# Kernel optimization log

Measured on AMD Instinct MI355X. Metric: run time of the kernel, lower is better.

Reference implementation:

```python
import jax, jax.numpy as jnp
import numpy as np

N = 20000   # nodes
E = 320000  # edges (avg degree 16)
K = 3       # Chebyshev order


def _glorot(key, shape):
    fan_in, fan_out = shape[-2], shape[-1]
    lim = (6.0 / (fan_in + fan_out)) ** 0.5
    return jax.random.uniform(key, shape, minval=-lim, maxval=lim, dtype=jnp.float32)


def setup_inputs() -> dict:
    key = jax.random.key(0)
    ks = jax.random.split(key, 8)
    v = jax.random.normal(ks[0], (N, 86), dtype=jnp.float32)
    edges = jax.random.randint(ks[1], (2, E), 0, N, dtype=jnp.int32)
    W1 = _glorot(ks[2], (K, 86, 128));  b1 = jnp.zeros((128,), jnp.float32)
    W2 = _glorot(ks[3], (K, 128, 256)); b2 = jnp.zeros((256,), jnp.float32)
    W3 = _glorot(ks[4], (K, 256, 512)); b3 = jnp.zeros((512,), jnp.float32)
    return {"v": v, "edges": edges, "W1": W1, "b1": b1,
            "W2": W2, "b2": b2, "W3": W3, "b3": b3}


def _cheb_norm(edges, n):
    # PyG ChebConv with sym norm, lambda_max=2: L_hat = L - I = -D^-1/2 A D^-1/2
    # (diagonal entries from get_laplacian (+1) and add_self_loops (-1) cancel).
    # Self loops are removed before computing the Laplacian -> mask them out.
    row, col = edges[0], edges[1]
    w = (row != col).astype(jnp.float32)
    deg = jax.ops.segment_sum(w, row, num_segments=n)
    dinv = jnp.where(deg > 0, jax.lax.rsqrt(jnp.maximum(deg, 1e-12)), 0.0)
    norm_w = -dinv[row] * w * dinv[col]  # [E]
    return row, col, norm_w


def _cheb_conv(x, row, col, norm_w, W, b):
    # W: [K, in, out]
    def prop(z):  # L_hat @ z via edge gather + segment scatter-add
        return jax.ops.segment_sum(norm_w[:, None] * z[col], row, num_segments=x.shape[0])
    Tx0 = x
    out = Tx0 @ W[0]
    Tx1 = prop(Tx0)
    out = out + Tx1 @ W[1]
    Tx2 = 2.0 * prop(Tx1) - Tx0
    out = out + Tx2 @ W[2]
    return out + b


def reference(v, edges, W1, b1, W2, b2, W3, b3):
    row, col, norm_w = _cheb_norm(edges, v.shape[0])
    nk = jax.random.key(42)
    x1 = jax.nn.relu(_cheb_conv(v, row, col, norm_w, W1, b1))
    x1 = x1 * jax.random.normal(jax.random.fold_in(nk, 1), x1.shape, x1.dtype)
    x2 = jax.nn.relu(_cheb_conv(x1, row, col, norm_w, W2, b2))
    x2 = x2 * jax.random.normal(jax.random.fold_in(nk, 2), x2.shape, x2.dtype)
    x3 = jax.nn.relu(_cheb_conv(x2, row, col, norm_w, W3, b3))
    x3 = x3 * jax.random.normal(jax.random.fold_in(nk, 3), x3.shape, x3.dtype)
    return (x1, x2, x3)
```

## Files before the change

kernel.cpp:

```cpp
#include <hip/hip_runtime.h>
#include <stdint.h>
#include <math.h>

#define DEV static __device__ __forceinline__

typedef __attribute__((ext_vector_type(8))) short bf16x8;
typedef __attribute__((ext_vector_type(4))) float f32x4;
typedef __attribute__((ext_vector_type(8))) unsigned short u16x8;

DEV uint32_t rotl32(uint32_t v, int d) { return (v << d) | (v >> (32 - d)); }

DEV void threefry2x32(uint32_t k0, uint32_t k1, uint32_t& x0, uint32_t& x1) {
  const uint32_t k2 = k0 ^ k1 ^ 0x1BD11BDAu;
  x0 += k0; x1 += k1;
#define TFR(R) { x0 += x1; x1 = rotl32(x1, R) ^ x0; }
  TFR(13) TFR(15) TFR(26) TFR(6)
  x0 += k1; x1 += k2 + 1u;
  TFR(17) TFR(29) TFR(16) TFR(24)
  x0 += k2; x1 += k0 + 2u;
  TFR(13) TFR(15) TFR(26) TFR(6)
  x0 += k0; x1 += k1 + 3u;
  TFR(17) TFR(29) TFR(16) TFR(24)
  x0 += k1; x1 += k2 + 4u;
  TFR(13) TFR(15) TFR(26) TFR(6)
  x0 += k2; x1 += k0 + 5u;
#undef TFR
}

DEV float erfinv_f32(float x) {
  float w = -log1pf(-x * x);
  float p;
  if (w < 5.0f) {
    w -= 2.5f;
    p = 2.81022636e-08f;
    p = fmaf(p, w, 3.43273939e-07f);
    p = fmaf(p, w, -3.5233877e-06f);
    p = fmaf(p, w, -4.39150654e-06f);
    p = fmaf(p, w, 0.00021858087f);
    p = fmaf(p, w, -0.00125372503f);
    p = fmaf(p, w, -0.00417768164f);
    p = fmaf(p, w, 0.246640727f);
    p = fmaf(p, w, 1.50140941f);
  } else {
    w = sqrtf(w) - 3.0f;
    p = -0.000200214257f;
    p = fmaf(p, w, 0.000100950558f);
    p = fmaf(p, w, 0.00134934322f);
    p = fmaf(p, w, -0.00367342844f);
    p = fmaf(p, w, 0.00573950773f);
    p = fmaf(p, w, -0.0076224613f);
    p = fmaf(p, w, 0.00943887047f);
    p = fmaf(p, w, 1.00167406f);
    p = fmaf(p, w, 2.83297682f);
  }
  return p * x;
}

DEV float normal_from_bits(uint32_t bits) {
  float f = __uint_as_float((bits >> 9) | 0x3F800000u) - 1.0f;
  const float lo = -0.99999994f;
  float u = fmaf(f, 2.0f, lo);
  u = fmaxf(u, lo);
  return 1.41421356f * erfinv_f32(u);
}

DEV unsigned short f2bf(float f) {
  uint32_t u = __float_as_uint(f);
  uint32_t r = u + 0x7FFFu + ((u >> 16) & 1u);
  return (unsigned short)(r >> 16);
}

DEV float bf2f(uint32_t h) { return __uint_as_float(h << 16); }

DEV float4 noise4(uint32_t f0, uint32_t f1, uint32_t i4) {
  uint32_t base = i4 * 4u;
  float4 r;
  { uint32_t a = 0u, b = base + 0u; threefry2x32(f0, f1, a, b); r.x = normal_from_bits(a ^ b); }
  { uint32_t a = 0u, b = base + 1u; threefry2x32(f0, f1, a, b); r.y = normal_from_bits(a ^ b); }
  { uint32_t a = 0u, b = base + 2u; threefry2x32(f0, f1, a, b); r.z = normal_from_bits(a ^ b); }
  { uint32_t a = 0u, b = base + 3u; threefry2x32(f0, f1, a, b); r.w = normal_from_bits(a ^ b); }
  return r;
}

DEV void noise_fill(unsigned short* __restrict__ nb, int total4, int fold,
                    int gbase, int gstride) {
  uint32_t f0k = 0u, f1k = (uint32_t)fold;
  threefry2x32(0u, 42u, f0k, f1k);
  for (int i4 = gbase; i4 < total4; i4 += gstride) {
    float4 r = noise4(f0k, f1k, (uint32_t)i4);
    uint2 u;
    u.x = (uint32_t)f2bf(r.x) | ((uint32_t)f2bf(r.y) << 16);
    u.y = (uint32_t)f2bf(r.z) | ((uint32_t)f2bf(r.w) << 16);
    *(uint2*)&nb[(size_t)i4 * 4] = u;
  }
}

__global__ void count_kernel(const int* __restrict__ rows, const int* __restrict__ cols,
                             int* __restrict__ counts, int* __restrict__ degs, int E) {
  int e = blockIdx.x * blockDim.x + threadIdx.x;
  if (e < E) {
    int r = rows[e];
    atomicAdd(&counts[r], 1);
    if (r != cols[e]) atomicAdd(&degs[r], 1);
  }
}

#define SCAN_T 1024
__global__ __launch_bounds__(SCAN_T) void scan_kernel(const int* __restrict__ counts,
                                                      int* __restrict__ row_ptr,
                                                      int* __restrict__ cursor, int N) {
  __shared__ int sa[SCAN_T], sb[SCAN_T];
  const int t = threadIdx.x;
  const int CH = (N + SCAN_T - 1) / SCAN_T;
  int base = t * CH;
  int psum = 0;
  for (int k = 0; k < CH; ++k) {
    int idx = base + k;
    if (idx < N) psum += counts[idx];
  }
  sa[t] = psum;
  __syncthreads();
  int* src = sa; int* dst = sb;
  for (int off = 1; off < SCAN_T; off <<= 1) {
    int v = src[t];
    if (t >= off) v += src[t - off];
    dst[t] = v;
    __syncthreads();
    int* tmp = src; src = dst; dst = tmp;
  }
  int running = src[t] - psum;
  for (int k = 0; k < CH; ++k) {
    int idx = base + k;
    if (idx < N) {
      row_ptr[idx] = running;
      cursor[idx] = running;
      running += counts[idx];
    }
  }
  if (t == SCAN_T - 1) row_ptr[N] = running;
}

__global__ void fill_kernel(const int* __restrict__ rows, const int* __restrict__ cols,
                            const int* __restrict__ degs, int* __restrict__ cursor,
                            float2* __restrict__ ecv, int E) {
  int e = blockIdx.x * blockDim.x + threadIdx.x;
  if (e < E) {
    int r = rows[e], c = cols[e];
    int dr = degs[r], dc = degs[c];
    float w = (r != c && dr > 0 && dc > 0) ? -rsqrtf((float)dr) * rsqrtf((float)dc) : 0.0f;
    int pos = atomicAdd(&cursor[r], 1);
    ecv[pos] = make_float2(__int_as_float(c), w);
  }
}

__global__ void prep_kernel(const float* __restrict__ v,
                            const float* __restrict__ W1, const float* __restrict__ W2,
                            const float* __restrict__ W3,
                            unsigned short* __restrict__ vb, unsigned short* __restrict__ wt1,
                            unsigned short* __restrict__ wt2, unsigned short* __restrict__ wt3,
                            unsigned short* __restrict__ nb1, int n1_total4, int N) {
  noise_fill(nb1, n1_total4, 1, blockIdx.x * 256 + threadIdx.x, gridDim.x * 256);

  int i = blockIdx.x * 256 + threadIdx.x;
  int nv = N * 96;
  if (i < nv) {
    int r = i / 96, k = i % 96;
    vb[i] = (k < 86) ? f2bf(v[(size_t)r * 86 + k]) : (unsigned short)0;
    return;
  }
  i -= nv;
  if (i < 3 * 128 * 96) {
    int k = i % 96, o = (i / 96) % 128, p = i / (96 * 128);
    float val = 0.0f;
    if (k < 86) {
      if (p == 0)      val = W1[((size_t)0 * 86 + k) * 128 + o] - W1[((size_t)2 * 86 + k) * 128 + o];
      else if (p == 1) val = W1[((size_t)1 * 86 + k) * 128 + o];
      else             val = 2.0f * W1[((size_t)2 * 86 + k) * 128 + o];
    }
    wt1[i] = (k < 86) ? f2bf(val) : (unsigned short)0;
    return;
  }
  i -= 3 * 128 * 96;
  if (i < 3 * 256 * 128) {
    int k = i % 128, o = (i / 128) % 256, p = i / (128 * 256);
    float val;
    if (p == 0)      val = W2[((size_t)0 * 128 + k) * 256 + o] - W2[((size_t)2 * 128 + k) * 256 + o];
    else if (p == 1) val = W2[((size_t)1 * 128 + k) * 256 + o];
    else             val = 2.0f * W2[((size_t)2 * 128 + k) * 256 + o];
    wt2[i] = f2bf(val);
    return;
  }
  i -= 3 * 256 * 128;
  if (i < 3 * 512 * 256) {
    int k = i % 256, o = (i / 256) % 512, p = i / (256 * 512);
    float val;
    if (p == 0)      val = W3[((size_t)0 * 256 + k) * 512 + o] - W3[((size_t)2 * 256 + k) * 512 + o];
    else if (p == 1) val = W3[((size_t)1 * 256 + k) * 512 + o];
    else             val = 2.0f * W3[((size_t)2 * 256 + k) * 512 + o];
    wt3[i] = f2bf(val);
  }
}

DEV void ld8(const unsigned short* __restrict__ base, size_t off, float* v) {
  uint4 u = *(const uint4*)(base + off);
  v[0] = bf2f(u.x & 0xffffu); v[1] = bf2f(u.x >> 16);
  v[2] = bf2f(u.y & 0xffffu); v[3] = bf2f(u.y >> 16);
  v[4] = bf2f(u.z & 0xffffu); v[5] = bf2f(u.z >> 16);
  v[6] = bf2f(u.w & 0xffffu); v[7] = bf2f(u.w >> 16);
}

template <int LPN, int NL>
__global__ __launch_bounds__(256) void gather_prop(
    const int* __restrict__ row_ptr, const float2* __restrict__ ecv,
    const unsigned short* __restrict__ xsrc, int sstride,
    unsigned short* __restrict__ outb, int N, int Fpad) {
  const int wave = threadIdx.x >> 6, lane = threadIdx.x & 63;
  const int sub = lane / LPN;
  const int fl = (lane - sub * LPN) * 8;
  const int node = (blockIdx.x * 4 + wave) * NL + sub;
  if (sub >= NL || node >= N) return;
  float acc[8] = {};
  const int s = row_ptr[node], e = row_ptr[node + 1];
  int j = s;
  for (; j + 8 <= e; j += 8) {
    float2 cw[8];
    float vv[8][8];
#pragma unroll
    for (int q = 0; q < 8; ++q) cw[q] = ecv[j + q];
#pragma unroll
    for (int q = 0; q < 8; ++q)
      ld8(xsrc, (size_t)__float_as_int(cw[q].x) * sstride + fl, vv[q]);
#pragma unroll
    for (int q = 0; q < 8; ++q)
#pragma unroll
      for (int z = 0; z < 8; ++z) acc[z] = fmaf(cw[q].y, vv[q][z], acc[z]);
  }
  for (; j + 2 <= e; j += 2) {
    float2 cw[2];
    float vv[2][8];
#pragma unroll
    for (int q = 0; q < 2; ++q) cw[q] = ecv[j + q];
#pragma unroll
    for (int q = 0; q < 2; ++q)
      ld8(xsrc, (size_t)__float_as_int(cw[q].x) * sstride + fl, vv[q]);
#pragma unroll
    for (int q = 0; q < 2; ++q)
#pragma unroll
      for (int z = 0; z < 8; ++z) acc[z] = fmaf(cw[q].y, vv[q][z], acc[z]);
  }
  for (; j < e; ++j) {
    float2 cw = ecv[j];
    float vv[8];
    ld8(xsrc, (size_t)__float_as_int(cw.x) * sstride + fl, vv);
#pragma unroll
    for (int z = 0; z < 8; ++z) acc[z] = fmaf(cw.y, vv[z], acc[z]);
  }
  uint4 u;
  u.x = (uint32_t)f2bf(acc[0]) | ((uint32_t)f2bf(acc[1]) << 16);
  u.y = (uint32_t)f2bf(acc[2]) | ((uint32_t)f2bf(acc[3]) << 16);
  u.z = (uint32_t)f2bf(acc[4]) | ((uint32_t)f2bf(acc[5]) << 16);
  u.w = (uint32_t)f2bf(acc[6]) | ((uint32_t)f2bf(acc[7]) << 16);
  *(uint4*)&outb[(size_t)node * Fpad + fl] = u;
}

template <int BM, int FPAD, int KS, int OB>
__global__ __launch_bounds__(512, 4) void gemm3_db(
    const unsigned short* __restrict__ A0, const unsigned short* __restrict__ A1,
    const unsigned short* __restrict__ A2,
    const unsigned short* __restrict__ Wt, const float* __restrict__ bias,
    const unsigned short* __restrict__ noise,
    int M, int MT, int O, float* __restrict__ out, unsigned short* __restrict__ outb,
    int obstride, unsigned short* __restrict__ nnext, int ntotal4, int nfold) {
  constexpr int BN = 128;
  constexpr int NSP = FPAD / KS;
  constexpr int NSTEP = 3 * NSP;
  constexpr int CPR = KS / 8;
  constexpr int LST = KS + 8;
  constexpr int NA = BM * CPR;
  constexpr int NB = BN * CPR;
  constexpr int ACH = (NA + 511) / 512;
  constexpr int BCH = (NB + 511) / 512;
  constexpr int MFR = BM / 32;
  constexpr int KK = KS / 32;

  const int flat = blockIdx.x;
  const int xcd = flat & 7, idx = flat >> 3;
  const int mtile = xcd + 8 * (idx / OB);
  const int obl = idx - (idx / OB) * OB;

  __shared__ unsigned short sA[2][BM * LST];
  __shared__ unsigned short sB[2][BN * LST];

  const int tid = threadIdx.x;

  if (mtile < MT) {
    const int bm = mtile * BM;
    const int bo = obl * BN;
    const int lane = tid & 63;
    const int wave = tid >> 6;
    const int wm = wave >> 2, wo = wave & 3;
    const int l15 = lane & 15;
    const int kg = (lane >> 4) * 8;

    f32x4 acc[MFR][2] = {};
    const unsigned short* As[3] = {A0, A1, A2};

    u16x8 ra0[ACH], rb0[BCH], ra1[ACH], rb1[BCH];

    auto issue = [&](int s, u16x8 (&ra)[ACH], u16x8 (&rb)[BCH]) {
      int p = s / NSP, k0 = (s % NSP) * KS;
      const unsigned short* __restrict__ A = As[p];
      const unsigned short* __restrict__ B = Wt + (size_t)p * O * FPAD;
#pragma unroll
      for (int c = 0; c < ACH; ++c) {
        int idx2 = tid + c * 512;
        if (NA % 512 == 0 || idx2 < NA) {
          int row = idx2 / CPR, ch = (idx2 % CPR) * 8;
          int gm = bm + row; if (gm >= M) gm = M - 1;
          ra[c] = *(const u16x8*)(A + (size_t)gm * FPAD + k0 + ch);
        }
      }
#pragma unroll
      for (int c = 0; c < BCH; ++c) {
        int idx2 = tid + c * 512;
        if (NB % 512 == 0 || idx2 < NB) {
          int row = idx2 / CPR, ch = (idx2 % CPR) * 8;
          rb[c] = *(const u16x8*)(B + (size_t)(bo + row) * FPAD + k0 + ch);
        }
      }
    };

    auto lds_write = [&](int buf, u16x8 (&ra)[ACH], u16x8 (&rb)[BCH]) {
#pragma unroll
      for (int c = 0; c < ACH; ++c) {
        int idx2 = tid + c * 512;
        if (NA % 512 == 0 || idx2 < NA) {
          int row = idx2 / CPR, ch = (idx2 % CPR) * 8;
          *(u16x8*)&sA[buf][row * LST + ch] = ra[c];
        }
      }
#pragma unroll
      for (int c = 0; c < BCH; ++c) {
        int idx2 = tid + c * 512;
        if (NB % 512 == 0 || idx2 < NB) {
          int row = idx2 / CPR, ch = (idx2 % CPR) * 8;
          *(u16x8*)&sB[buf][row * LST + ch] = rb[c];
        }
      }
    };

    auto compute = [&](int buf) {
#pragma unroll
      for (int kk = 0; kk < KK; ++kk) {
        bf16x8 af[MFR], bfr[2];
#pragma unroll
        for (int mi = 0; mi < MFR; ++mi)
          af[mi] = *(const bf16x8*)&sA[buf][(wm * (BM / 2) + mi * 16 + l15) * LST + kk * 32 + kg];
#pragma unroll
        for (int ni = 0; ni < 2; ++ni)
          bfr[ni] = *(const bf16x8*)&sB[buf][(wo * 32 + ni * 16 + l15) * LST + kk * 32 + kg];
#pragma unroll
        for (int mi = 0; mi < MFR; ++mi)
#pragma unroll
          for (int ni = 0; ni < 2; ++ni)
            acc[mi][ni] = __builtin_amdgcn_mfma_f32_16x16x32_bf16(af[mi], bfr[ni], acc[mi][ni], 0, 0, 0);
      }
    };

    issue(0, ra0, rb0);
    issue(1, ra1, rb1);
    lds_write(0, ra0, rb0);
    __syncthreads();

#pragma unroll
    for (int s = 0; s < NSTEP; ++s) {
      if ((s & 1) == 0) {
        if (s + 2 < NSTEP) issue(s + 2, ra0, rb0);
        compute(s & 1);
        if (s + 1 < NSTEP) { lds_write((s + 1) & 1, ra1, rb1); __syncthreads(); }
      } else {
        if (s + 2 < NSTEP) issue(s + 2, ra1, rb1);
        compute(s & 1);
        if (s + 1 < NSTEP) { lds_write((s + 1) & 1, ra0, rb0); __syncthreads(); }
      }
    }

    const int r0 = (lane >> 4) * 4;
#pragma unroll
    for (int mi = 0; mi < MFR; ++mi) {
#pragma unroll
      for (int r = 0; r < 4; ++r) {
        int gm = bm + wm * (BM / 2) + mi * 16 + r0 + r;
        if (gm >= M) continue;
#pragma unroll
        for (int ni = 0; ni < 2; ++ni) {
          int go = bo + wo * 32 + ni * 16 + l15;
          float vv = acc[mi][ni][r] + bias[go];
          vv = vv > 0.0f ? vv : 0.0f;
          float res = vv * bf2f((uint32_t)noise[(size_t)gm * O + go]);
          out[(size_t)gm * O + go] = res;
          if (outb) outb[(size_t)gm * obstride + go] = f2bf(res);
        }
      }
    }
  }

  if (nnext)
    noise_fill(nnext, ntotal4, nfold, blockIdx.x * 512 + tid, gridDim.x * 512);
}

extern "C" void kernel_launch(void* const* d_in, const int* in_sizes, int n_in,
                              void* d_out, int out_size, void* d_ws, size_t ws_size,
                              hipStream_t stream) {
  const float* v    = (const float*)d_in[0];
  const int*  edges = (const int*)d_in[1];
  const float* W1 = (const float*)d_in[2];
  const float* b1 = (const float*)d_in[3];
  const float* W2 = (const float*)d_in[4];
  const float* b2 = (const float*)d_in[5];
  const float* W3 = (const float*)d_in[6];
  const float* b3 = (const float*)d_in[7];
  float* out = (float*)d_out;

  const int N = in_sizes[0] / 86;
  const int E = in_sizes[1] / 2;
  const int* rows = edges;
  const int* cols = edges + E;

  uintptr_t cur = (uintptr_t)d_ws;
  auto alloc = [&](size_t bytes) {
    cur = (cur + 15) & ~(uintptr_t)15;
    void* p = (void*)cur;
    cur += bytes;
    return p;
  };
  float2* ecv          = (float2*)alloc((size_t)E * 8);
  int* counts          = (int*)alloc((size_t)N * 4);
  int* degs            = (int*)alloc((size_t)N * 4);
  int* row_ptr         = (int*)alloc((size_t)(N + 1) * 4);
  int* cursor          = (int*)alloc((size_t)N * 4);
  unsigned short* tx1b = (unsigned short*)alloc((size_t)N * 256 * 2);
  unsigned short* tx2b = (unsigned short*)alloc((size_t)N * 256 * 2);
  unsigned short* vb   = (unsigned short*)alloc((size_t)N * 96 * 2);
  unsigned short* x1b  = (unsigned short*)alloc((size_t)N * 128 * 2);
  unsigned short* x2b  = (unsigned short*)alloc((size_t)N * 256 * 2);
  unsigned short* wt1  = (unsigned short*)alloc((size_t)3 * 128 * 96 * 2);
  unsigned short* wt2  = (unsigned short*)alloc((size_t)3 * 256 * 128 * 2);
  unsigned short* wt3  = (unsigned short*)alloc((size_t)3 * 512 * 256 * 2);
  unsigned short* nb2  = (unsigned short*)alloc((size_t)N * 256 * 2);
  unsigned short* nb3  = (unsigned short*)alloc((size_t)N * 512 * 2);
  unsigned short* nb1  = nb3;

  float* x1 = out;
  float* x2 = x1 + (size_t)N * 128;
  float* x3 = x2 + (size_t)N * 256;

  hipMemsetAsync(counts, 0, (size_t)2 * N * sizeof(int), stream);
  count_kernel<<<(E + 255) / 256, 256, 0, stream>>>(rows, cols, counts, degs, E);
  scan_kernel<<<1, SCAN_T, 0, stream>>>(counts, row_ptr, cursor, N);
  fill_kernel<<<(E + 255) / 256, 256, 0, stream>>>(rows, cols, degs, cursor, ecv, E);
  {
    int total = N * 96 + 3 * 128 * 96 + 3 * 256 * 128 + 3 * 512 * 256;
    prep_kernel<<<(total + 255) / 256, 256, 0, stream>>>(v, W1, W2, W3, vb, wt1, wt2, wt3,
                                                         nb1, N * 128 / 4, N);
  }

  {
    int pb = (N + 15) / 16;
    gather_prop<12, 4><<<pb, 256, 0, stream>>>(row_ptr, ecv, vb, 96, tx1b, N, 96);
    gather_prop<12, 4><<<pb, 256, 0, stream>>>(row_ptr, ecv, tx1b, 96, tx2b, N, 96);
    int mt = (N + 63) / 64;
    int grid = 8 * ((mt + 7) / 8) * 1;
    gemm3_db<64, 96, 32, 1><<<grid, 512, 0, stream>>>(vb, tx1b, tx2b, wt1, b1, nb1,
                                                      N, mt, 128, x1, x1b, 128,
                                                      nb2, N * 256 / 4, 2);
  }
  {
    int pb = (N + 15) / 16;
    gather_prop<16, 4><<<pb, 256, 0, stream>>>(row_ptr, ecv, x1b, 128, tx1b, N, 128);
    gather_prop<16, 4><<<pb, 256, 0, stream>>>(row_ptr, ecv, tx1b, 128, tx2b, N, 128);
    int mt = (N + 127) / 128;
    int grid = 8 * ((mt + 7) / 8) * 2;
    gemm3_db<128, 128, 64, 2><<<grid, 512, 0, stream>>>(x1b, tx1b, tx2b, wt2, b2, nb2,
                                                        N, mt, 256, x2, x2b, 256,
                                                        nb3, N * 512 / 4, 3);
  }
  {
    int pb = (N + 7) / 8;
    gather_prop<32, 2><<<pb, 256, 0, stream>>>(row_ptr, ecv, x2b, 256, tx1b, N, 256);
    gather_prop<32, 2><<<pb, 256, 0, stream>>>(row_ptr, ecv, tx1b, 256, tx2b, N, 256);
    int mt = (N + 127) / 128;
    int grid = 8 * ((mt + 7) / 8) * 4;
    gemm3_db<128, 256, 64, 4><<<grid, 512, 0, stream>>>(x2b, tx1b, tx2b, wt3, b3, nb3,
                                                        N, mt, 512, x3, nullptr, 0,
                                                        nullptr, 0, 0);
  }
}
```

Before: 416.4 us.

## Move noise generation into gather kernels and slice gathers by feature per XCD

Noise generation for each layer moves out of prep and the previous GEMM's tail into the two memory-bound gather kernels of that layer, each filling half the buffer. The intent is to overlap the ALU-heavy threefry work with gather memory latency and shorten the GEMMs. The layer-2 and layer-3 gathers get a new kernel that maps 64-feature slices to XCDs, so each XCD's L2 holds only a column slice of the source features. The risk is extra ALU load on the gathers, plus occupancy effects.

Measured after the change: 369.0 us. 11.4% less time.

```diff
diff --git a/kernel.cpp b/kernel.cpp
--- a/kernel.cpp
+++ b/kernel.cpp
@@ -82,11 +82,11 @@
   return r;
 }
 
-DEV void noise_fill(unsigned short* __restrict__ nb, int total4, int fold,
+DEV void noise_fill(unsigned short* __restrict__ nb, int n4_begin, int n4_end, int fold,
                     int gbase, int gstride) {
   uint32_t f0k = 0u, f1k = (uint32_t)fold;
   threefry2x32(0u, 42u, f0k, f1k);
-  for (int i4 = gbase; i4 < total4; i4 += gstride) {
+  for (int i4 = n4_begin + gbase; i4 < n4_end; i4 += gstride) {
     float4 r = noise4(f0k, f1k, (uint32_t)i4);
     uint2 u;
     u.x = (uint32_t)f2bf(r.x) | ((uint32_t)f2bf(r.y) << 16);
@@ -158,9 +158,7 @@
                             const float* __restrict__ W3,
                             unsigned short* __restrict__ vb, unsigned short* __restrict__ wt1,
                             unsigned short* __restrict__ wt2, unsigned short* __restrict__ wt3,
-                            unsigned short* __restrict__ nb1, int n1_total4, int N) {
-  noise_fill(nb1, n1_total4, 1, blockIdx.x * 256 + threadIdx.x, gridDim.x * 256);
-
+                            int N) {
   int i = blockIdx.x * 256 + threadIdx.x;
   int nv = N * 96;
   if (i < nv) {
@@ -209,17 +207,9 @@
   v[6] = bf2f(u.w & 0xffffu); v[7] = bf2f(u.w >> 16);
 }
 
-template <int LPN, int NL>
-__global__ __launch_bounds__(256) void gather_prop(
-    const int* __restrict__ row_ptr, const float2* __restrict__ ecv,
-    const unsigned short* __restrict__ xsrc, int sstride,
-    unsigned short* __restrict__ outb, int N, int Fpad) {
-  const int wave = threadIdx.x >> 6, lane = threadIdx.x & 63;
-  const int sub = lane / LPN;
-  const int fl = (lane - sub * LPN) * 8;
-  const int node = (blockIdx.x * 4 + wave) * NL + sub;
-  if (sub >= NL || node >= N) return;
-  float acc[8] = {};
+DEV void gather_node(const int* __restrict__ row_ptr, const float2* __restrict__ ecv,
+                     const unsigned short* __restrict__ xsrc, int sstride, int fl,
+                     int node, float* acc) {
   const int s = row_ptr[node], e = row_ptr[node + 1];
   int j = s;
   for (; j + 8 <= e; j += 8) {
@@ -255,12 +245,57 @@
 #pragma unroll
     for (int z = 0; z < 8; ++z) acc[z] = fmaf(cw.y, vv[z], acc[z]);
   }
+}
+
+DEV void store8(unsigned short* __restrict__ outb, size_t ob, const float* acc) {
   uint4 u;
   u.x = (uint32_t)f2bf(acc[0]) | ((uint32_t)f2bf(acc[1]) << 16);
   u.y = (uint32_t)f2bf(acc[2]) | ((uint32_t)f2bf(acc[3]) << 16);
   u.z = (uint32_t)f2bf(acc[4]) | ((uint32_t)f2bf(acc[5]) << 16);
   u.w = (uint32_t)f2bf(acc[6]) | ((uint32_t)f2bf(acc[7]) << 16);
-  *(uint4*)&outb[(size_t)node * Fpad + fl] = u;
+  *(uint4*)&outb[ob] = u;
+}
+
+template <int LPN, int NL, int FOLD>
+__global__ __launch_bounds__(256) void gather_prop(
+    const int* __restrict__ row_ptr, const float2* __restrict__ ecv,
+    const unsigned short* __restrict__ xsrc, int sstride,
+    unsigned short* __restrict__ outb, int N, int Fpad,
+    unsigned short* __restrict__ nbuf, int n4_begin, int n4_end) {
+  const int wave = threadIdx.x >> 6, lane = threadIdx.x & 63;
+  const int sub = lane / LPN;
+  const int fl = (lane - sub * LPN) * 8;
+  const int node = (blockIdx.x * 4 + wave) * NL + sub;
+  if (sub < NL && node < N && fl < Fpad) {
+    float acc[8] = {};
+    gather_node(row_ptr, ecv, xsrc, sstride, fl, node, acc);
+    store8(outb, (size_t)node * Fpad + fl, acc);
+  }
+  noise_fill(nbuf, n4_begin, n4_end, FOLD, blockIdx.x * 256 + (int)threadIdx.x, gridDim.x * 256);
+}
+
+template <int G, int FOLD>
+__global__ __launch_bounds__(256) void gather_prop_sl(
+    const int* __restrict__ row_ptr, const float2* __restrict__ ecv,
+    const unsigned short* __restrict__ xsrc, int sstride,
+    unsigned short* __restrict__ outb, int N, int Fpad, int NBK,
+    unsigned short* __restrict__ nbuf, int n4_begin, int n4_end) {
+  const int flat = blockIdx.x;
+  const int xcd = flat & 7, j = flat >> 3;
+  const int slice = xcd / G;
+  const int nb = j * G + (xcd % G);
+  if (nb < NBK) {
+    const int wave = threadIdx.x >> 6, lane = threadIdx.x & 63;
+    const int sub = lane >> 3;
+    const int fl = slice * 64 + (lane & 7) * 8;
+    const int node = nb * 32 + wave * 8 + sub;
+    if (node < N) {
+      float acc[8] = {};
+      gather_node(row_ptr, ecv, xsrc, sstride, fl, node, acc);
+      store8(outb, (size_t)node * Fpad + fl, acc);
+    }
+  }
+  noise_fill(nbuf, n4_begin, n4_end, FOLD, flat * 256 + (int)threadIdx.x, gridDim.x * 256);
 }
 
 template <int BM, int FPAD, int KS, int OB>
@@ -270,7 +305,7 @@
     const unsigned short* __restrict__ Wt, const float* __restrict__ bias,
     const unsigned short* __restrict__ noise,
     int M, int MT, int O, float* __restrict__ out, unsigned short* __restrict__ outb,
-    int obstride, unsigned short* __restrict__ nnext, int ntotal4, int nfold) {
+    int obstride) {
   constexpr int BN = 128;
   constexpr int NSP = FPAD / KS;
   constexpr int NSTEP = 3 * NSP;
@@ -287,126 +322,121 @@
   const int xcd = flat & 7, idx = flat >> 3;
   const int mtile = xcd + 8 * (idx / OB);
   const int obl = idx - (idx / OB) * OB;
+  if (mtile >= MT) return;
+  const int bm = mtile * BM;
+  const int bo = obl * BN;
 
   __shared__ unsigned short sA[2][BM * LST];
   __shared__ unsigned short sB[2][BN * LST];
 
   const int tid = threadIdx.x;
-
-  if (mtile < MT) {
-    const int bm = mtile * BM;
-    const int bo = obl * BN;
-    const int lane = tid & 63;
-    const int wave = tid >> 6;
-    const int wm = wave >> 2, wo = wave & 3;
-    const int l15 = lane & 15;
-    const int kg = (lane >> 4) * 8;
-
-    f32x4 acc[MFR][2] = {};
-    const unsigned short* As[3] = {A0, A1, A2};
-
-    u16x8 ra0[ACH], rb0[BCH], ra1[ACH], rb1[BCH];
-
-    auto issue = [&](int s, u16x8 (&ra)[ACH], u16x8 (&rb)[BCH]) {
-      int p = s / NSP, k0 = (s % NSP) * KS;
-      const unsigned short* __restrict__ A = As[p];
-      const unsigned short* __restrict__ B = Wt + (size_t)p * O * FPAD;
-#pragma unroll
-      for (int c = 0; c < ACH; ++c) {
-        int idx2 = tid + c * 512;
-        if (NA % 512 == 0 || idx2 < NA) {
-          int row = idx2 / CPR, ch = (idx2 % CPR) * 8;
-          int gm = bm + row; if (gm >= M) gm = M - 1;
-          ra[c] = *(const u16x8*)(A + (size_t)gm * FPAD + k0 + ch);
-        }
+  const int lane = tid & 63;
+  const int wave = tid >> 6;
+  const int wm = wave >> 2, wo = wave & 3;
+  const int l15 = lane & 15;
+  const int kg = (lane >> 4) * 8;
+
+  f32x4 acc[MFR][2] = {};
+  const unsigned short* As[3] = {A0, A1, A2};
+
+  u16x8 ra0[ACH], rb0[BCH], ra1[ACH], rb1[BCH];
+
+  auto issue = [&](int s, u16x8 (&ra)[ACH], u16x8 (&rb)[BCH]) {
+    int p = s / NSP, k0 = (s % NSP) * KS;
+    const unsigned short* __restrict__ A = As[p];
+    const unsigned short* __restrict__ B = Wt + (size_t)p * O * FPAD;
+#pragma unroll
+    for (int c = 0; c < ACH; ++c) {
+      int idx2 = tid + c * 512;
+      if (NA % 512 == 0 || idx2 < NA) {
+        int row = idx2 / CPR, ch = (idx2 % CPR) * 8;
+        int gm = bm + row; if (gm >= M) gm = M - 1;
+        ra[c] = *(const u16x8*)(A + (size_t)gm * FPAD + k0 + ch);
       }
-#pragma unroll
-      for (int c = 0; c < BCH; ++c) {
-        int idx2 = tid + c * 512;
-        if (NB % 512 == 0 || idx2 < NB) {
-          int row = idx2 / CPR, ch = (idx2 % CPR) * 8;
-          rb[c] = *(const u16x8*)(B + (size_t)(bo + row) * FPAD + k0 + ch);
-        }
+    }
+#pragma unroll
+    for (int c = 0; c < BCH; ++c) {
+      int idx2 = tid + c * 512;
+      if (NB % 512 == 0 || idx2 < NB) {
+        int row = idx2 / CPR, ch = (idx2 % CPR) * 8;
+        rb[c] = *(const u16x8*)(B + (size_t)(bo + row) * FPAD + k0 + ch);
       }
-    };
-
-    auto lds_write = [&](int buf, u16x8 (&ra)[ACH], u16x8 (&rb)[BCH]) {
-#pragma unroll
-      for (int c = 0; c < ACH; ++c) {
-        int idx2 = tid + c * 512;
-        if (NA % 512 == 0 || idx2 < NA) {
-          int row = idx2 / CPR, ch = (idx2 % CPR) * 8;
-          *(u16x8*)&sA[buf][row * LST + ch] = ra[c];
-        }
+    }
+  };
+
+  auto lds_write = [&](int buf, u16x8 (&ra)[ACH], u16x8 (&rb)[BCH]) {
+#pragma unroll
+    for (int c = 0; c < ACH; ++c) {
+      int idx2 = tid + c * 512;
+      if (NA % 512 == 0 || idx2 < NA) {
+        int row = idx2 / CPR, ch = (idx2 % CPR) * 8;
+        *(u16x8*)&sA[buf][row * LST + ch] = ra[c];
       }
-#pragma unroll
-      for (int c = 0; c < BCH; ++c) {
-        int idx2 = tid + c * 512;
-        if (NB % 512 == 0 || idx2 < NB) {
-          int row = idx2 / CPR, ch = (idx2 % CPR) * 8;
-          *(u16x8*)&sB[buf][row * LST + ch] = rb[c];
-        }
+    }
+#pragma unroll
+    for (int c = 0; c < BCH; ++c) {
+      int idx2 = tid + c * 512;
+      if (NB % 512 == 0 || idx2 < NB) {
+        int row = idx2 / CPR, ch = (idx2 % CPR) * 8;
+        *(u16x8*)&sB[buf][row * LST + ch] = rb[c];
       }
-    };
-
-    auto compute = [&](int buf) {
-#pragma unroll
-      for (int kk = 0; kk < KK; ++kk) {
-        bf16x8 af[MFR], bfr[2];
-#pragma unroll
-        for (int mi = 0; mi < MFR; ++mi)
-          af[mi] = *(const bf16x8*)&sA[buf][(wm * (BM / 2) + mi * 16 + l15) * LST + kk * 32 + kg];
+    }
+  };
+
+  auto compute = [&](int buf) {
+#pragma unroll
+    for (int kk = 0; kk < KK; ++kk) {
+      bf16x8 af[MFR], bfr[2];
+#pragma unroll
+      for (int mi = 0; mi < MFR; ++mi)
+        af[mi] = *(const bf16x8*)&sA[buf][(wm * (BM / 2) + mi * 16 + l15) * LST + kk * 32 + kg];
+#pragma unroll
+      for (int ni = 0; ni < 2; ++ni)
+        bfr[ni] = *(const bf16x8*)&sB[buf][(wo * 32 + ni * 16 + l15) * LST + kk * 32 + kg];
+#pragma unroll
+      for (int mi = 0; mi < MFR; ++mi)
 #pragma unroll
         for (int ni = 0; ni < 2; ++ni)
-          bfr[ni] = *(const bf16x8*)&sB[buf][(wo * 32 + ni * 16 + l15) * LST + kk * 32 + kg];
-#pragma unroll
-        for (int mi = 0; mi < MFR; ++mi)
-#pragma unroll
-          for (int ni = 0; ni < 2; ++ni)
-            acc[mi][ni] = __builtin_amdgcn_mfma_f32_16x16x32_bf16(af[mi], bfr[ni], acc[mi][ni], 0, 0, 0);
+          acc[mi][ni] = __builtin_amdgcn_mfma_f32_16x16x32_bf16(af[mi], bfr[ni], acc[mi][ni], 0, 0, 0);
+    }
+  };
+
+  issue(0, ra0, rb0);
+  issue(1, ra1, rb1);
+  lds_write(0, ra0, rb0);
+  __syncthreads();
+
+#pragma unroll
+  for (int s = 0; s < NSTEP; ++s) {
+    if ((s & 1) == 0) {
+      if (s + 2 < NSTEP) issue(s + 2, ra0, rb0);
+      compute(s & 1);
+      if (s + 1 < NSTEP) { lds_write((s + 1) & 1, ra1, rb1); __syncthreads(); }
+    } else {
+      if (s + 2 < NSTEP) issue(s + 2, ra1, rb1);
+      compute(s & 1);
+      if (s + 1 < NSTEP) { lds_write((s + 1) & 1, ra0, rb0); __syncthreads(); }
+    }
+  }
+
+  const int r0 = (lane >> 4) * 4;
+#pragma unroll
+  for (int mi = 0; mi < MFR; ++mi) {
+#pragma unroll
+    for (int r = 0; r < 4; ++r) {
+      int gm = bm + wm * (BM / 2) + mi * 16 + r0 + r;
+      if (gm >= M) continue;
+#pragma unroll
+      for (int ni = 0; ni < 2; ++ni) {
+        int go = bo + wo * 32 + ni * 16 + l15;
+        float vv = acc[mi][ni][r] + bias[go];
+        vv = vv > 0.0f ? vv : 0.0f;
+        float res = vv * bf2f((uint32_t)noise[(size_t)gm * O + go]);
+        out[(size_t)gm * O + go] = res;
+        if (outb) outb[(size_t)gm * obstride + go] = f2bf(res);
       }
-    };
-
-    issue(0, ra0, rb0);
-    issue(1, ra1, rb1);
-    lds_write(0, ra0, rb0);
-    __syncthreads();
-
-#pragma unroll
-    for (int s = 0; s < NSTEP; ++s) {
-      if ((s & 1) == 0) {
-        if (s + 2 < NSTEP) issue(s + 2, ra0, rb0);
-        compute(s & 1);
-        if (s + 1 < NSTEP) { lds_write((s + 1) & 1, ra1, rb1); __syncthreads(); }
-      } else {
-        if (s + 2 < NSTEP) issue(s + 2, ra1, rb1);
-        compute(s & 1);
-        if (s + 1 < NSTEP) { lds_write((s + 1) & 1, ra0, rb0); __syncthreads(); }
-      }
-    }
-
-    const int r0 = (lane >> 4) * 4;
-#pragma unroll
-    for (int mi = 0; mi < MFR; ++mi) {
-#pragma unroll
-      for (int r = 0; r < 4; ++r) {
-        int gm = bm + wm * (BM / 2) + mi * 16 + r0 + r;
-        if (gm >= M) continue;
-#pragma unroll
-        for (int ni = 0; ni < 2; ++ni) {
-          int go = bo + wo * 32 + ni * 16 + l15;
-          float vv = acc[mi][ni][r] + bias[go];
-          vv = vv > 0.0f ? vv : 0.0f;
-          float res = vv * bf2f((uint32_t)noise[(size_t)gm * O + go]);
-          out[(size_t)gm * O + go] = res;
-          if (outb) outb[(size_t)gm * obstride + go] = f2bf(res);
-        }
-      }
-    }
-  }
-
-  if (nnext)
-    noise_fill(nnext, ntotal4, nfold, blockIdx.x * 512 + tid, gridDim.x * 512);
+    }
+  }
 }
 
 extern "C" void kernel_launch(void* const* d_in, const int* in_sizes, int n_in,
@@ -461,38 +491,39 @@
   fill_kernel<<<(E + 255) / 256, 256, 0, stream>>>(rows, cols, degs, cursor, ecv, E);
   {
     int total = N * 96 + 3 * 128 * 96 + 3 * 256 * 128 + 3 * 512 * 256;
-    prep_kernel<<<(total + 255) / 256, 256, 0, stream>>>(v, W1, W2, W3, vb, wt1, wt2, wt3,
-                                                         nb1, N * 128 / 4, N);
-  }
+    prep_kernel<<<(total + 255) / 256, 256, 0, stream>>>(v, W1, W2, W3, vb, wt1, wt2, wt3, N);
+  }
+
+  const int NBK = (N + 31) / 32;
 
   {
     int pb = (N + 15) / 16;
-    gather_prop<12, 4><<<pb, 256, 0, stream>>>(row_ptr, ecv, vb, 96, tx1b, N, 96);
-    gather_prop<12, 4><<<pb, 256, 0, stream>>>(row_ptr, ecv, tx1b, 96, tx2b, N, 96);
+    int t4 = N * 128 / 4, h4 = t4 / 2;
+    gather_prop<12, 4, 1><<<pb, 256, 0, stream>>>(row_ptr, ecv, vb, 96, tx1b, N, 96, nb1, 0, h4);
+    gather_prop<12, 4, 1><<<pb, 256, 0, stream>>>(row_ptr, ecv, tx1b, 96, tx2b, N, 96, nb1, h4, t4);
     int mt = (N + 63) / 64;
     int grid = 8 * ((mt + 7) / 8) * 1;
     gemm3_db<64, 96, 32, 1><<<grid, 512, 0, stream>>>(vb, tx1b, tx2b, wt1, b1, nb1,
-                                                      N, mt, 128, x1, x1b, 128,
-                                                      nb2, N * 256 / 4, 2);
+                                                      N, mt, 128, x1, x1b, 128);
   }
   {
-    int pb = (N + 15) / 16;
-    gather_prop<16, 4><<<pb, 256, 0, stream>>>(row_ptr, ecv, x1b, 128, tx1b, N, 128);
-    gather_prop<16, 4><<<pb, 256, 0, stream>>>(row_ptr, ecv, tx1b, 128, tx2b, N, 128);
+    int pgrid = 8 * ((NBK + 3) / 4);
+    int t4 = N * 256 / 4, h4 = t4 / 2;
+    gather_prop_sl<4, 2><<<pgrid, 256, 0, stream>>>(row_ptr, ecv, x1b, 128, tx1b, N, 128, NBK, nb2, 0, h4);
+    gather_prop_sl<4, 2><<<pgrid, 256, 0, stream>>>(row_ptr, ecv, tx1b, 128, tx2b, N, 128, NBK, nb2, h4, t4);
     int mt = (N + 127) / 128;
     int grid = 8 * ((mt + 7) / 8) * 2;
     gemm3_db<128, 128, 64, 2><<<grid, 512, 0, stream>>>(x1b, tx1b, tx2b, wt2, b2, nb2,
-                                                        N, mt, 256, x2, x2b, 256,
-                                                        nb3, N * 512 / 4, 3);
+                                                        N, mt, 256, x2, x2b, 256);
   }
   {
-    int pb = (N + 7) / 8;
-    gather_prop<32, 2><<<pb, 256, 0, stream>>>(row_ptr, ecv, x2b, 256, tx1b, N, 256);
-    gather_prop<32, 2><<<pb, 256, 0, stream>>>(row_ptr, ecv, tx1b, 256, tx2b, N, 256);
+    int pgrid = 8 * ((NBK + 1) / 2);
+    int t4 = N * 512 / 4, h4 = t4 / 2;
+    gather_prop_sl<2, 3><<<pgrid, 256, 0, stream>>>(row_ptr, ecv, x2b, 256, tx1b, N, 256, NBK, nb3, 0, h4);
+    gather_prop_sl<2, 3><<<pgrid, 256, 0, stream>>>(row_ptr, ecv, tx1b, 256, tx2b, N, 256, NBK, nb3, h4, t4);
     int mt = (N + 127) / 128;
     int grid = 8 * ((mt + 7) / 8) * 4;
     gemm3_db<128, 256, 64, 4><<<grid, 512, 0, stream>>>(x2b, tx1b, tx2b, wt3, b3, nb3,
-                                                        N, mt, 512, x3, nullptr, 0,
-                                                        nullptr, 0, 0);
-  }
-}
+                                                        N, mt, 512, x3, nullptr, 0);
+  }
+}
```

## Move next-layer noise generation into dedicated extra GEMM blocks

Applied to the files above, without the earlier changes.

Before, every GEMM block ran the next layer's threefry noise fill after finishing its tile. Now the GEMM grid gets KN=384 extra blocks that only generate noise, while the tile blocks return right after their epilogue. This is meant to let noise generation overlap with the MFMA work instead of lengthening every tile block's tail. The gather kernel is also refactored into helper functions, with an added fl>=Fpad guard. The cost is extra blocks competing for CUs, and the noise work is now spread over fewer threads.

Result: faster. 386.0 us (-7.3%).

```diff
diff --git a/kernel.cpp b/kernel.cpp
--- a/kernel.cpp
+++ b/kernel.cpp
@@ -7,6 +7,8 @@
 typedef __attribute__((ext_vector_type(8))) short bf16x8;
 typedef __attribute__((ext_vector_type(4))) float f32x4;
 typedef __attribute__((ext_vector_type(8))) unsigned short u16x8;
+typedef __attribute__((ext_vector_type(2))) unsigned int u32x2;
+typedef __attribute__((ext_vector_type(4))) unsigned int u32x4;
 
 DEV uint32_t rotl32(uint32_t v, int d) { return (v << d) | (v >> (32 - d)); }
 
@@ -82,16 +84,16 @@
   return r;
 }
 
-DEV void noise_fill(unsigned short* __restrict__ nb, int total4, int fold,
+DEV void noise_fill(unsigned short* __restrict__ nb, int n4_end, int fold,
                     int gbase, int gstride) {
   uint32_t f0k = 0u, f1k = (uint32_t)fold;
   threefry2x32(0u, 42u, f0k, f1k);
-  for (int i4 = gbase; i4 < total4; i4 += gstride) {
+  for (int i4 = gbase; i4 < n4_end; i4 += gstride) {
     float4 r = noise4(f0k, f1k, (uint32_t)i4);
-    uint2 u;
+    u32x2 u;
     u.x = (uint32_t)f2bf(r.x) | ((uint32_t)f2bf(r.y) << 16);
     u.y = (uint32_t)f2bf(r.z) | ((uint32_t)f2bf(r.w) << 16);
-    *(uint2*)&nb[(size_t)i4 * 4] = u;
+    *(u32x2*)&nb[(size_t)i4 * 4] = u;
   }
 }
 
@@ -159,7 +161,7 @@
                             unsigned short* __restrict__ vb, unsigned short* __restrict__ wt1,
                             unsigned short* __restrict__ wt2, unsigned short* __restrict__ wt3,
                             unsigned short* __restrict__ nb1, int n1_total4, int N) {
-  noise_fill(nb1, n1_total4, 1, blockIdx.x * 256 + threadIdx.x, gridDim.x * 256);
+  noise_fill(nb1, n1_total4, 1, blockIdx.x * 256 + (int)threadIdx.x, gridDim.x * 256);
 
   int i = blockIdx.x * 256 + threadIdx.x;
   int nv = N * 96;
@@ -209,6 +211,55 @@
   v[6] = bf2f(u.w & 0xffffu); v[7] = bf2f(u.w >> 16);
 }
 
+DEV void gather_node(const int* __restrict__ row_ptr, const float2* __restrict__ ecv,
+                     const unsigned short* __restrict__ xsrc, int sstride, int fl,
+                     int node, float* acc) {
+  const int s = row_ptr[node], e = row_ptr[node + 1];
+  int j = s;
+  for (; j + 8 <= e; j += 8) {
+    float2 cw[8];
+    float vv[8][8];
+#pragma unroll
+    for (int q = 0; q < 8; ++q) cw[q] = ecv[j + q];
+#pragma unroll
+    for (int q = 0; q < 8; ++q)
+      ld8(xsrc, (size_t)__float_as_int(cw[q].x) * sstride + fl, vv[q]);
+#pragma unroll
+    for (int q = 0; q < 8; ++q)
+#pragma unroll
+      for (int z = 0; z < 8; ++z) acc[z] = fmaf(cw[q].y, vv[q][z], acc[z]);
+  }
+  for (; j + 2 <= e; j += 2) {
+    float2 cw[2];
+    float vv[2][8];
+#pragma unroll
+    for (int q = 0; q < 2; ++q) cw[q] = ecv[j + q];
+#pragma unroll
+    for (int q = 0; q < 2; ++q)
+      ld8(xsrc, (size_t)__float_as_int(cw[q].x) * sstride + fl, vv[q]);
+#pragma unroll
+    for (int q = 0; q < 2; ++q)
+#pragma unroll
+      for (int z = 0; z < 8; ++z) acc[z] = fmaf(cw[q].y, vv[q][z], acc[z]);
+  }
+  for (; j < e; ++j) {
+    float2 cw = ecv[j];
+    float vv[8];
+    ld8(xsrc, (size_t)__float_as_int(cw.x) * sstride + fl, vv);
+#pragma unroll
+    for (int z = 0; z < 8; ++z) acc[z] = fmaf(cw.y, vv[z], acc[z]);
+  }
+}
+
+DEV void store8(unsigned short* __restrict__ outb, size_t ob, const float* acc) {
+  u32x4 u;
+  u.x = (uint32_t)f2bf(acc[0]) | ((uint32_t)f2bf(acc[1]) << 16);
+  u.y = (uint32_t)f2bf(acc[2]) | ((uint32_t)f2bf(acc[3]) << 16);
+  u.z = (uint32_t)f2bf(acc[4]) | ((uint32_t)f2bf(acc[5]) << 16);
+  u.w = (uint32_t)f2bf(acc[6]) | ((uint32_t)f2bf(acc[7]) << 16);
+  *(u32x4*)&outb[ob] = u;
+}
+
 template <int LPN, int NL>
 __global__ __launch_bounds__(256) void gather_prop(
     const int* __restrict__ row_ptr, const float2* __restrict__ ecv,
@@ -218,49 +269,10 @@
   const int sub = lane / LPN;
   const int fl = (lane - sub * LPN) * 8;
   const int node = (blockIdx.x * 4 + wave) * NL + sub;
-  if (sub >= NL || node >= N) return;
+  if (sub >= NL || node >= N || fl >= Fpad) return;
   float acc[8] = {};
-  const int s = row_ptr[node], e = row_ptr[node + 1];
-  int j = s;
-  for (; j + 8 <= e; j += 8) {
-    float2 cw[8];
-    float vv[8][8];
-#pragma unroll
-    for (int q = 0; q < 8; ++q) cw[q] = ecv[j + q];
-#pragma unroll
-    for (int q = 0; q < 8; ++q)
-      ld8(xsrc, (size_t)__float_as_int(cw[q].x) * sstride + fl, vv[q]);
-#pragma unroll
-    for (int q = 0; q < 8; ++q)
-#pragma unroll
-      for (int z = 0; z < 8; ++z) acc[z] = fmaf(cw[q].y, vv[q][z], acc[z]);
-  }
-  for (; j + 2 <= e; j += 2) {
-    float2 cw[2];
-    float vv[2][8];
-#pragma unroll
-    for (int q = 0; q < 2; ++q) cw[q] = ecv[j + q];
-#pragma unroll
-    for (int q = 0; q < 2; ++q)
-      ld8(xsrc, (size_t)__float_as_int(cw[q].x) * sstride + fl, vv[q]);
-#pragma unroll
-    for (int q = 0; q < 2; ++q)
-#pragma unroll
-      for (int z = 0; z < 8; ++z) acc[z] = fmaf(cw[q].y, vv[q][z], acc[z]);
-  }
-  for (; j < e; ++j) {
-    float2 cw = ecv[j];
-    float vv[8];
-    ld8(xsrc, (size_t)__float_as_int(cw.x) * sstride + fl, vv);
-#pragma unroll
-    for (int z = 0; z < 8; ++z) acc[z] = fmaf(cw.y, vv[z], acc[z]);
-  }
-  uint4 u;
-  u.x = (uint32_t)f2bf(acc[0]) | ((uint32_t)f2bf(acc[1]) << 16);
-  u.y = (uint32_t)f2bf(acc[2]) | ((uint32_t)f2bf(acc[3]) << 16);
-  u.z = (uint32_t)f2bf(acc[4]) | ((uint32_t)f2bf(acc[5]) << 16);
-  u.w = (uint32_t)f2bf(acc[6]) | ((uint32_t)f2bf(acc[7]) << 16);
-  *(uint4*)&outb[(size_t)node * Fpad + fl] = u;
+  gather_node(row_ptr, ecv, xsrc, sstride, fl, node, acc);
+  store8(outb, (size_t)node * Fpad + fl, acc);
 }
 
 template <int BM, int FPAD, int KS, int OB>
@@ -270,7 +282,7 @@
     const unsigned short* __restrict__ Wt, const float* __restrict__ bias,
     const unsigned short* __restrict__ noise,
     int M, int MT, int O, float* __restrict__ out, unsigned short* __restrict__ outb,
-    int obstride, unsigned short* __restrict__ nnext, int ntotal4, int nfold) {
+    int obstride, int GG, unsigned short* __restrict__ nnext, int ntotal4, int nfold) {
   constexpr int BN = 128;
   constexpr int NSP = FPAD / KS;
   constexpr int NSTEP = 3 * NSP;
@@ -284,129 +296,133 @@
   constexpr int KK = KS / 32;
 
   const int flat = blockIdx.x;
+  if (flat >= GG) {
+    if (nnext) {
+      int rank = flat - GG;
+      int stride = ((int)gridDim.x - GG) * 512;
+      noise_fill(nnext, ntotal4, nfold, rank * 512 + (int)threadIdx.x, stride);
+    }
+    return;
+  }
+
   const int xcd = flat & 7, idx = flat >> 3;
   const int mtile = xcd + 8 * (idx / OB);
   const int obl = idx - (idx / OB) * OB;
+  if (mtile >= MT) return;
+  const int bm = mtile * BM;
+  const int bo = obl * BN;
 
   __shared__ unsigned short sA[2][BM * LST];
   __shared__ unsigned short sB[2][BN * LST];
 
   const int tid = threadIdx.x;
-
-  if (mtile < MT) {
-    const int bm = mtile * BM;
-    const int bo = obl * BN;
-    const int lane = tid & 63;
-    const int wave = tid >> 6;
-    const int wm = wave >> 2, wo = wave & 3;
-    const int l15 = lane & 15;
-    const int kg = (lane >> 4) * 8;
-
-    f32x4 acc[MFR][2] = {};
-    const unsigned short* As[3] = {A0, A1, A2};
-
-    u16x8 ra0[ACH], rb0[BCH], ra1[ACH], rb1[BCH];
-
-    auto issue = [&](int s, u16x8 (&ra)[ACH], u16x8 (&rb)[BCH]) {
-      int p = s / NSP, k0 = (s % NSP) * KS;
-      const unsigned short* __restrict__ A = As[p];
-      const unsigned short* __restrict__ B = Wt + (size_t)p * O * FPAD;
-#pragma unroll
-      for (int c = 0; c < ACH; ++c) {
-        int idx2 = tid + c * 512;
-        if (NA % 512 == 0 || idx2 < NA) {
-          int row = idx2 / CPR, ch = (idx2 % CPR) * 8;
-          int gm = bm + row; if (gm >= M) gm = M - 1;
-          ra[c] = *(const u16x8*)(A + (size_t)gm * FPAD + k0 + ch);
-        }
+  const int lane = tid & 63;
+  const int wave = tid >> 6;
+  const int wm = wave >> 2, wo = wave & 3;
+  const int l15 = lane & 15;
+  const int kg = (lane >> 4) * 8;
+
+  f32x4 acc[MFR][2] = {};
+  const unsigned short* As[3] = {A0, A1, A2};
+
+  u16x8 ra0[ACH], rb0[BCH], ra1[ACH], rb1[BCH];
+
+  auto issue = [&](int s, u16x8 (&ra)[ACH], u16x8 (&rb)[BCH]) {
+    int p = s / NSP, k0 = (s % NSP) * KS;
+    const unsigned short* __restrict__ A = As[p];
+    const unsigned short* __restrict__ B = Wt + (size_t)p * O * FPAD;
+#pragma unroll
+    for (int c = 0; c < ACH; ++c) {
+      int idx2 = tid + c * 512;
+      if (NA % 512 == 0 || idx2 < NA) {
+        int row = idx2 / CPR, ch = (idx2 % CPR) * 8;
+        int gm = bm + row; if (gm >= M) gm = M - 1;
+        ra[c] = *(const u16x8*)(A + (size_t)gm * FPAD + k0 + ch);
       }
-#pragma unroll
-      for (int c = 0; c < BCH; ++c) {
-        int idx2 = tid + c * 512;
-        if (NB % 512 == 0 || idx2 < NB) {
-          int row = idx2 / CPR, ch = (idx2 % CPR) * 8;
-          rb[c] = *(const u16x8*)(B + (size_t)(bo + row) * FPAD + k0 + ch);
-        }
+    }
+#pragma unroll
+    for (int c = 0; c < BCH; ++c) {
+      int idx2 = tid + c * 512;
+      if (NB % 512 == 0 || idx2 < NB) {
+        int row = idx2 / CPR, ch = (idx2 % CPR) * 8;
+        rb[c] = *(const u16x8*)(B + (size_t)(bo + row) * FPAD + k0 + ch);
       }
-    };
-
-    auto lds_write = [&](int buf, u16x8 (&ra)[ACH], u16x8 (&rb)[BCH]) {
-#pragma unroll
-      for (int c = 0; c < ACH; ++c) {
-        int idx2 = tid + c * 512;
-        if (NA % 512 == 0 || idx2 < NA) {
-          int row = idx2 / CPR, ch = (idx2 % CPR) * 8;
-          *(u16x8*)&sA[buf][row * LST + ch] = ra[c];
-        }
+    }
+  };
+
+  auto lds_write = [&](int buf, u16x8 (&ra)[ACH], u16x8 (&rb)[BCH]) {
+#pragma unroll
+    for (int c = 0; c < ACH; ++c) {
+      int idx2 = tid + c * 512;
+      if (NA % 512 == 0 || idx2 < NA) {
+        int row = idx2 / CPR, ch = (idx2 % CPR) * 8;
+        *(u16x8*)&sA[buf][row * LST + ch] = ra[c];
       }
-#pragma unroll
-      for (int c = 0; c < BCH; ++c) {
-        int idx2 = tid + c * 512;
-        if (NB % 512 == 0 || idx2 < NB) {
-          int row = idx2 / CPR, ch = (idx2 % CPR) * 8;
-          *(u16x8*)&sB[buf][row * LST + ch] = rb[c];
-        }
+    }
+#pragma unroll
+    for (int c = 0; c < BCH; ++c) {
+      int idx2 = tid + c * 512;
+      if (NB % 512 == 0 || idx2 < NB) {
+        int row = idx2 / CPR, ch = (idx2 % CPR) * 8;
+        *(u16x8*)&sB[buf][row * LST + ch] = rb[c];
       }
-    };
-
-    auto compute = [&](int buf) {
-#pragma unroll
-      for (int kk = 0; kk < KK; ++kk) {
-        bf16x8 af[MFR], bfr[2];
-#pragma unroll
-        for (int mi = 0; mi < MFR; ++mi)
-          af[mi] = *(const bf16x8*)&sA[buf][(wm * (BM / 2) + mi * 16 + l15) * LST + kk * 32 + kg];
+    }
+  };
+
+  auto compute = [&](int buf) {
+#pragma unroll
+    for (int kk = 0; kk < KK; ++kk) {
+      bf16x8 af[MFR], bfr[2];
+#pragma unroll
+      for (int mi = 0; mi < MFR; ++mi)
+        af[mi] = *(const bf16x8*)&sA[buf][(wm * (BM / 2) + mi * 16 + l15) * LST + kk * 32 + kg];
+#pragma unroll
+      for (int ni = 0; ni < 2; ++ni)
+        bfr[ni] = *(const bf16x8*)&sB[buf][(wo * 32 + ni * 16 + l15) * LST + kk * 32 + kg];
+#pragma unroll
+      for (int mi = 0; mi < MFR; ++mi)
 #pragma unroll
         for (int ni = 0; ni < 2; ++ni)
-          bfr[ni] = *(const bf16x8*)&sB[buf][(wo * 32 + ni * 16 + l15) * LST + kk * 32 + kg];
-#pragma unroll
-        for (int mi = 0; mi < MFR; ++mi)
-#pragma unroll
-          for (int ni = 0; ni < 2; ++ni)
-            acc[mi][ni] = __builtin_amdgcn_mfma_f32_16x16x32_bf16(af[mi], bfr[ni], acc[mi][ni], 0, 0, 0);
+          acc[mi][ni] = __builtin_amdgcn_mfma_f32_16x16x32_bf16(af[mi], bfr[ni], acc[mi][ni], 0, 0, 0);
+    }
+  };
+
+  issue(0, ra0, rb0);
+  issue(1, ra1, rb1);
+  lds_write(0, ra0, rb0);
+  __syncthreads();
+
+#pragma unroll
+  for (int s = 0; s < NSTEP; ++s) {
+    if ((s & 1) == 0) {
+      if (s + 2 < NSTEP) issue(s + 2, ra0, rb0);
+      compute(s & 1);
+      if (s + 1 < NSTEP) { lds_write((s + 1) & 1, ra1, rb1); __syncthreads(); }
+    } else {
+      if (s + 2 < NSTEP) issue(s + 2, ra1, rb1);
+      compute(s & 1);
+      if (s + 1 < NSTEP) { lds_write((s + 1) & 1, ra0, rb0); __syncthreads(); }
+    }
+  }
+
+  const int r0 = (lane >> 4) * 4;
+#pragma unroll
+  for (int mi = 0; mi < MFR; ++mi) {
+#pragma unroll
+    for (int r = 0; r < 4; ++r) {
+      int gm = bm + wm * (BM / 2) + mi * 16 + r0 + r;
+      if (gm >= M) continue;
+#pragma unroll
+      for (int ni = 0; ni < 2; ++ni) {
+        int go = bo + wo * 32 + ni * 16 + l15;
+        float vv = acc[mi][ni][r] + bias[go];
+        vv = vv > 0.0f ? vv : 0.0f;
+        float res = vv * bf2f((uint32_t)noise[(size_t)gm * O + go]);
+        out[(size_t)gm * O + go] = res;
+        if (outb) outb[(size_t)gm * obstride + go] = f2bf(res);
       }
-    };
-
-    issue(0, ra0, rb0);
-    issue(1, ra1, rb1);
-    lds_write(0, ra0, rb0);
-    __syncthreads();
-
-#pragma unroll
-    for (int s = 0; s < NSTEP; ++s) {
-      if ((s & 1) == 0) {
-        if (s + 2 < NSTEP) issue(s + 2, ra0, rb0);
-        compute(s & 1);
-        if (s + 1 < NSTEP) { lds_write((s + 1) & 1, ra1, rb1); __syncthreads(); }
-      } else {
-        if (s + 2 < NSTEP) issue(s + 2, ra1, rb1);
-        compute(s & 1);
-        if (s + 1 < NSTEP) { lds_write((s + 1) & 1, ra0, rb0); __syncthreads(); }
-      }
-    }
-
-    const int r0 = (lane >> 4) * 4;
-#pragma unroll
-    for (int mi = 0; mi < MFR; ++mi) {
-#pragma unroll
-      for (int r = 0; r < 4; ++r) {
-        int gm = bm + wm * (BM / 2) + mi * 16 + r0 + r;
-        if (gm >= M) continue;
-#pragma unroll
-        for (int ni = 0; ni < 2; ++ni) {
-          int go = bo + wo * 32 + ni * 16 + l15;
-          float vv = acc[mi][ni][r] + bias[go];
-          vv = vv > 0.0f ? vv : 0.0f;
-          float res = vv * bf2f((uint32_t)noise[(size_t)gm * O + go]);
-          out[(size_t)gm * O + go] = res;
-          if (outb) outb[(size_t)gm * obstride + go] = f2bf(res);
-        }
-      }
-    }
-  }
-
-  if (nnext)
-    noise_fill(nnext, ntotal4, nfold, blockIdx.x * 512 + tid, gridDim.x * 512);
+    }
+  }
 }
 
 extern "C" void kernel_launch(void* const* d_in, const int* in_sizes, int n_in,
@@ -465,34 +481,36 @@
                                                          nb1, N * 128 / 4, N);
   }
 
+  const int KN = 384;
+
   {
     int pb = (N + 15) / 16;
     gather_prop<12, 4><<<pb, 256, 0, stream>>>(row_ptr, ecv, vb, 96, tx1b, N, 96);
     gather_prop<12, 4><<<pb, 256, 0, stream>>>(row_ptr, ecv, tx1b, 96, tx2b, N, 96);
     int mt = (N + 63) / 64;
-    int grid = 8 * ((mt + 7) / 8) * 1;
-    gemm3_db<64, 96, 32, 1><<<grid, 512, 0, stream>>>(vb, tx1b, tx2b, wt1, b1, nb1,
-                                                      N, mt, 128, x1, x1b, 128,
-                                                      nb2, N * 256 / 4, 2);
+    int GG = 8 * ((mt + 7) / 8) * 1;
+    gemm3_db<64, 96, 32, 1><<<GG + KN, 512, 0, stream>>>(vb, tx1b, tx2b, wt1, b1, nb1,
+                                                         N, mt, 128, x1, x1b, 128,
+                                                         GG, nb2, N * 256 / 4, 2);
   }
   {
     int pb = (N + 15) / 16;
     gather_prop<16, 4><<<pb, 256, 0, stream>>>(row_ptr, ecv, x1b, 128, tx1b, N, 128);
     gather_prop<16, 4><<<pb, 256, 0, stream>>>(row_ptr, ecv, tx1b, 128, tx2b, N, 128);
     int mt = (N + 127) / 128;
-    int grid = 8 * ((mt + 7) / 8) * 2;
-    gemm3_db<128, 128, 64, 2><<<grid, 512, 0, stream>>>(x1b, tx1b, tx2b, wt2, b2, nb2,
-                                                        N, mt, 256, x2, x2b, 256,
-                                                        nb3, N * 512 / 4, 3);
+    int GG = 8 * ((mt + 7) / 8) * 2;
+    gemm3_db<128, 128, 64, 2><<<GG + KN, 512, 0, stream>>>(x1b, tx1b, tx2b, wt2, b2, nb2,
+                                                           N, mt, 256, x2, x2b, 256,
+                                                           GG, nb3, N * 512 / 4, 3);
   }
   {
     int pb = (N + 7) / 8;
     gather_prop<32, 2><<<pb, 256, 0, stream>>>(row_ptr, ecv, x2b, 256, tx1b, N, 256);
     gather_prop<32, 2><<<pb, 256, 0, stream>>>(row_ptr, ecv, tx1b, 256, tx2b, N, 256);
     int mt = (N + 127) / 128;
-    int grid = 8 * ((mt + 7) / 8) * 4;
-    gemm3_db<128, 256, 64, 4><<<grid, 512, 0, stream>>>(x2b, tx1b, tx2b, wt3, b3, nb3,
-                                                        N, mt, 512, x3, nullptr, 0,
-                                                        nullptr, 0, 0);
-  }
-}
+    int GG = 8 * ((mt + 7) / 8) * 4;
+    gemm3_db<128, 256, 64, 4><<<GG, 512, 0, stream>>>(x2b, tx1b, tx2b, wt3, b3, nb3,
+                                                      N, mt, 512, x3, nullptr, 0,
+                                                      GG, nullptr, 0, 0);
+  }
+}
```
